# Kernel optimization log

Hardware: AMD Instinct MI355X
Metric: run time of the kernel (lower is better)

The kernel has to match this reference:

```python
import jax, jax.numpy as jnp
import numpy as np

N = 100000   # nodes
R = 8        # relations
E = 150000   # edges per relation
D_IN = 128
D_OUT = 128
B = 2        # num_bases


def setup_inputs() -> dict:
    key = jax.random.key(0)
    ks = jax.random.split(key, 7)
    return {
        "x": jax.random.normal(ks[0], (N, D_IN), dtype=jnp.float32),
        "src": jax.random.randint(ks[1], (R, E), 0, N, dtype=jnp.int32),
        "dst": jax.random.randint(ks[2], (R, E), 0, N, dtype=jnp.int32),
        "basis_coeff": jax.random.normal(ks[3], (R, B), dtype=jnp.float32),
        "bases": jax.random.normal(ks[4], (B, D_IN, D_OUT), dtype=jnp.float32) * 0.05,
        "loop_weight": jax.random.normal(ks[5], (D_IN, D_OUT), dtype=jnp.float32) * 0.05,
        "h_bias": jax.random.normal(ks[6], (D_OUT,), dtype=jnp.float32) * 0.01,
    }


def reference(x, src, dst, basis_coeff, bases, loop_weight, h_bias):
    n = x.shape[0]
    # basis-decomposed per-relation weights: [R, D_IN, D_OUT]
    weight = jnp.einsum('rb,bio->rio', basis_coeff, bases)
    # gather src features per relation: [R, E, D_IN]
    msgs = x[src]
    # scatter-add onto dst nodes per relation (SpMM aggregate): [R, N, D_IN]
    agg = jax.vmap(lambda m, d: jax.ops.segment_sum(m, d, num_segments=n))(msgs, dst)
    # right normalization: divide by in-degree (clamped to 1), as in DGL GraphConv norm='right'
    ones = jnp.ones(src.shape[1], dtype=x.dtype)
    deg = jax.vmap(lambda d: jax.ops.segment_sum(ones, d, num_segments=n))(dst)
    agg = agg / jnp.clip(deg, 1.0)[..., None]
    # per-relation weight then sum across relations (HeteroGraphConv 'sum' agg)
    h = jnp.einsum('rni,rio->no', agg, weight)
    # self-loop + bias + activation (dropout = 0.0, eval)
    h = h + x @ loop_weight + h_bias
    return jax.nn.relu(h)
```

## Files before the change

### kernel.cpp

```cpp
#include <hip/hip_runtime.h>
#include <hip/hip_fp16.h>


#define DFEAT 128
#define NREL 8
#define ALDA 264
#define ECAP 1024

typedef __attribute__((ext_vector_type(8))) short bf16x8;
typedef __attribute__((ext_vector_type(4))) float f32x4;
typedef __attribute__((ext_vector_type(2))) float f32x2;

__device__ __forceinline__ ushort f2bf(float f) {
    unsigned u = __float_as_uint(f);
    u += 0x7FFF + ((u >> 16) & 1);
    return (ushort)(u >> 16);
}
__device__ __forceinline__ float bflo(unsigned u) { return __uint_as_float(u << 16); }
__device__ __forceinline__ float bfhi(unsigned u) { return __uint_as_float(u & 0xFFFF0000u); }
__device__ __forceinline__ unsigned pack2bf(float lo, float hi) {
    return (unsigned)f2bf(lo) | ((unsigned)f2bf(hi) << 16);
}

__global__ void fused_pre(const int* __restrict__ dst, int* __restrict__ deg,
                          ushort* __restrict__ rank,
                          const float* __restrict__ x, ushort* __restrict__ xb,
                          const float* __restrict__ bases, const float* __restrict__ loopw,
                          ushort* __restrict__ w2T,
                          int RE, int E, int N, int n4) {
    const int stride = gridDim.x * blockDim.x;
    const int t0 = blockIdx.x * blockDim.x + threadIdx.x;
    for (int i = t0; i < RE; i += stride) {
        int r = i / E;
        int d = dst[i];
        rank[i] = (ushort)atomicAdd(&deg[r * N + d], 1);
    }
    for (int i = t0; i < n4; i += stride) {
        float4 v = ((const float4*)x)[i];
        ushort4 o;
        o.x = f2bf(v.x); o.y = f2bf(v.y); o.z = f2bf(v.z); o.w = f2bf(v.w);
        ((ushort4*)xb)[i] = o;
    }
    for (int i = t0; i < 128 * 384; i += stride) {
        int j = i / 384, k = i % 384;
        float v = (k < 256) ? bases[(k >> 7) * DFEAT * DFEAT + (k & 127) * DFEAT + j]
                            : loopw[(k - 256) * DFEAT + j];
        w2T[i] = f2bf(v);
    }
}

__global__ void scan_block_sums(const int* __restrict__ deg, int* __restrict__ cnt,
                                int* __restrict__ bsums, int N) {
    __shared__ int sdata[256];
    int b = blockIdx.x, t = threadIdx.x;
    int idx = b * 256 + t;
    int sum = 0;
    if (idx < N) {
        #pragma unroll
        for (int r = 0; r < NREL; ++r) sum += deg[r * N + idx];
        cnt[idx] = sum;
    }
    sdata[t] = sum; __syncthreads();
    for (int s = 128; s > 0; s >>= 1) {
        if (t < s) sdata[t] += sdata[t + s];
        __syncthreads();
    }
    if (t == 0) bsums[b] = sdata[0];
}

__global__ void scan_write(const int* __restrict__ cnt, const int* __restrict__ bsums,
                           const int* __restrict__ deg,
                           int* __restrict__ rowStart, unsigned* __restrict__ packed,
                           int N) {
    __shared__ int sdata[256];
    int b = blockIdx.x, t = threadIdx.x;

    int part = 0;
    for (int k = t; k < b; k += 256) part += bsums[k];
    sdata[t] = part; __syncthreads();
    for (int s = 128; s > 0; s >>= 1) {
        if (t < s) sdata[t] += sdata[t + s];
        __syncthreads();
    }
    const int boff = sdata[0];
    __syncthreads();

    int idx = b * 256 + t;
    int c = (idx < N) ? cnt[idx] : 0;
    sdata[t] = c; __syncthreads();
    for (int off = 1; off < 256; off <<= 1) {
        int x = 0;
        if (t >= off) x = sdata[t - off];
        __syncthreads();
        if (t >= off) sdata[t] += x;
        __syncthreads();
    }
    int excl = sdata[t] - c;
    if (idx < N) {
        int rs = boff + excl;
        rowStart[idx] = rs;
        int pre = 0;
        #pragma unroll
        for (int r = 0; r < NREL; ++r) {
            int dv = deg[r * N + idx];
            packed[r * N + idx] = ((unsigned)(rs + pre) << 11) | (unsigned)dv;
            pre += dv;
        }
    }
}

__global__ void fill_kernel(const int* __restrict__ src, const int* __restrict__ dst,
                            const float* __restrict__ coeff,
                            const ushort* __restrict__ rank,
                            const unsigned* __restrict__ packed,
                            uint2* __restrict__ recs, int RE, int E, int N) {
    int idx = blockIdx.x * blockDim.x + threadIdx.x;
    if (idx >= RE) return;
    int r = idx / E;
    int d = dst[idx];
    unsigned p = packed[r * N + d];
    int pos = (int)(p >> 11) + (int)rank[idx];
    float inv = 1.0f / (float)(p & 2047u);
    __half2 hc = __floats2half2_rn(coeff[2 * r] * inv, coeff[2 * r + 1] * inv);
    uint2 rec;
    rec.x = (unsigned)src[idx];
    rec.y = *(unsigned*)&hc;
    recs[pos] = rec;
}

__global__ __launch_bounds__(256, 5) void gather_gemm(
    const uint2* __restrict__ recs, const int* __restrict__ rowStart,
    const ushort* __restrict__ xb,
    const ushort* __restrict__ w2T, const float* __restrict__ bias,
    float* __restrict__ out, int N, int RE) {
    __shared__ __align__(16) ushort agg[32 * ALDA];
    __shared__ __align__(16) uint2 recsL[ECAP];
    __shared__ int rsl[33];
    const int tid = threadIdx.x;
    const int wave = tid >> 6, lane = tid & 63;
    const int row0 = blockIdx.x * 32;

    if (tid < 33) {
        int d = row0 + tid;
        rsl[tid] = (d < N) ? rowStart[d] : RE;
    }
    __syncthreads();
    const int e0 = rsl[0];
    const int cntE = rsl[32] - e0;
    const bool fits = (cntE <= ECAP);
    {
        const int lim = fits ? cntE : 0;
        for (int k = tid; k < lim; k += 256)
            recsL[k] = recs[e0 + k];
    }
    __syncthreads();

    {
        const int qw = tid >> 4;
        const int h  = tid & 15;

        auto gatherNode = [&](int i, auto getRec) {
            const int s   = rsl[i] - e0;
            const int len = rsl[i + 1] - rsl[i];
            f32x2 A0 = {0.f,0.f}, A1 = {0.f,0.f}, A2 = {0.f,0.f}, A3 = {0.f,0.f};
            f32x2 B0 = {0.f,0.f}, B1 = {0.f,0.f}, B2 = {0.f,0.f}, B3 = {0.f,0.f};
            if (len > 0) {
                const int last = s + len - 1;
                for (int k = 0; k < len; k += 8) {
                    uint2 rc[8];
                    #pragma unroll
                    for (int j = 0; j < 8; ++j) {
                        int li = s + k + j;
                        rc[j] = getRec(li <= last ? li : last);
                    }
                    uint4 u[8];
                    #pragma unroll
                    for (int j = 0; j < 8; ++j)
                        u[j] = *(const uint4*)(xb + (size_t)rc[j].x * DFEAT + h * 8);
                    #pragma unroll
                    for (int j = 0; j < 8; ++j) {
                        bool v = (k + j) < len;
                        __half2 hc = *(__half2*)&rc[j].y;
                        float c0 = v ? __low2float(hc) : 0.f;
                        float c1 = v ? __high2float(hc) : 0.f;
                        f32x2 cc0 = {c0, c0}, cc1 = {c1, c1};
                        uint4 uu = u[j];
                        f32x2 f01 = {bflo(uu.x), bfhi(uu.x)};
                        f32x2 f23 = {bflo(uu.y), bfhi(uu.y)};
                        f32x2 f45 = {bflo(uu.z), bfhi(uu.z)};
                        f32x2 f67 = {bflo(uu.w), bfhi(uu.w)};
                        A0 += cc0 * f01; A1 += cc0 * f23; A2 += cc0 * f45; A3 += cc0 * f67;
                        B0 += cc1 * f01; B1 += cc1 * f23; B2 += cc1 * f45; B3 += cc1 * f67;
                    }
                }
            }
            uint4 w0, w1;
            w0.x = pack2bf(A0.x, A0.y); w0.y = pack2bf(A1.x, A1.y);
            w0.z = pack2bf(A2.x, A2.y); w0.w = pack2bf(A3.x, A3.y);
            w1.x = pack2bf(B0.x, B0.y); w1.y = pack2bf(B1.x, B1.y);
            w1.z = pack2bf(B2.x, B2.y); w1.w = pack2bf(B3.x, B3.y);
            *(uint4*)(agg + i * ALDA + h * 8)       = w0;
            *(uint4*)(agg + i * ALDA + 128 + h * 8) = w1;
        };

        if (fits) {
            #pragma unroll
            for (int p = 0; p < 2; ++p)
                gatherNode(qw + p * 16, [&](int li) { return recsL[li]; });
        } else {
            #pragma unroll
            for (int p = 0; p < 2; ++p)
                gatherNode(qw + p * 16, [&](int li) { return recs[e0 + li]; });
        }
    }
    __syncthreads();

    const int quad = lane >> 4, l16 = lane & 15;
    int arow[2];
    #pragma unroll
    for (int m = 0; m < 2; ++m) {
        int r = row0 + m * 16 + l16;
        arow[m] = (r < N) ? r : 0;
    }

    f32x4 zero = {0.f, 0.f, 0.f, 0.f};
    f32x4 acc[2][2] = {{zero, zero}, {zero, zero}};

    #pragma unroll
    for (int kt = 0; kt < 3; ++kt) {
        bf16x8 bq[4][2];
        #pragma unroll
        for (int t = 0; t < 4; ++t)
            #pragma unroll
            for (int g = 0; g < 2; ++g)
                bq[t][g] = *(const bf16x8*)(w2T + (size_t)(wave * 32 + g * 16 + l16) * 384
                                            + kt * 128 + t * 32 + quad * 8);
        #pragma unroll
        for (int m = 0; m < 2; ++m) {
            #pragma unroll
            for (int t = 0; t < 4; ++t) {
                bf16x8 a;
                if (kt < 2)
                    a = *(const bf16x8*)(agg + (m * 16 + l16) * ALDA + kt * 128 + t * 32 + quad * 8);
                else
                    a = *(const bf16x8*)(xb + (size_t)arow[m] * DFEAT + t * 32 + quad * 8);
                acc[m][0] = __builtin_amdgcn_mfma_f32_16x16x32_bf16(a, bq[t][0], acc[m][0], 0, 0, 0);
                acc[m][1] = __builtin_amdgcn_mfma_f32_16x16x32_bf16(a, bq[t][1], acc[m][1], 0, 0, 0);
            }
        }
    }

    #pragma unroll
    for (int g = 0; g < 2; ++g) {
        int c = wave * 32 + g * 16 + l16;
        float bv = bias[c];
        #pragma unroll
        for (int m = 0; m < 2; ++m) {
            #pragma unroll
            for (int reg = 0; reg < 4; ++reg) {
                int grow = row0 + m * 16 + quad * 4 + reg;
                if (grow < N)
                    out[(size_t)grow * DFEAT + c] = fmaxf(acc[m][g][reg] + bv, 0.f);
            }
        }
    }
}

extern "C" void kernel_launch(void* const* d_in, const int* in_sizes, int n_in,
                              void* d_out, int out_size, void* d_ws, size_t ws_size,
                              hipStream_t stream) {
    const float* x     = (const float*)d_in[0];
    const int*   src   = (const int*)  d_in[1];
    const int*   dst   = (const int*)  d_in[2];
    const float* coeff = (const float*)d_in[3];
    const float* bases = (const float*)d_in[4];
    const float* loopw = (const float*)d_in[5];
    const float* bias  = (const float*)d_in[6];
    float* out = (float*)d_out;

    const int N  = in_sizes[0] / DFEAT;
    const int RE = in_sizes[1];
    const int B  = in_sizes[4] / (DFEAT * DFEAT);
    const int R  = in_sizes[3] / B;
    const int E  = RE / R;
    const int NB = (N + 255) / 256;
    const int n4 = N * 32;

    char* ws = (char*)d_ws;
    size_t off = 0;
    auto alloc = [&](size_t bytes) { void* p = ws + off; off = (off + bytes + 255) & ~(size_t)255; return p; };
    int*      deg      = (int*)     alloc((size_t)R * N * sizeof(int));
    ushort*   rank     = (ushort*)  alloc((size_t)RE * sizeof(ushort));
    unsigned* packed   = (unsigned*)alloc((size_t)R * N * sizeof(unsigned));
    int*      cnt      = (int*)     alloc((size_t)N * sizeof(int));
    int*      rowStart = (int*)     alloc((size_t)N * sizeof(int));
    int*      bsums    = (int*)     alloc((size_t)NB * sizeof(int));
    ushort*   w2T      = (ushort*)  alloc((size_t)128 * 384 * sizeof(ushort));
    ushort*   xb       = (ushort*)  alloc((size_t)N * DFEAT * sizeof(ushort));
    uint2*    recs     = (uint2*)   alloc((size_t)RE * sizeof(uint2));

    hipMemsetAsync(deg, 0, (size_t)R * N * sizeof(int), stream);
    fused_pre<<<4096, 256, 0, stream>>>(dst, deg, rank, x, xb, bases, loopw, w2T,
                                        RE, E, N, n4);
    scan_block_sums<<<NB, 256, 0, stream>>>(deg, cnt, bsums, N);
    scan_write<<<NB, 256, 0, stream>>>(cnt, bsums, deg, rowStart, packed, N);
    fill_kernel<<<(RE + 255) / 256, 256, 0, stream>>>(src, dst, coeff, rank, packed,
                                                      recs, RE, E, N);
    gather_gemm<<<(N + 31) / 32, 256, 0, stream>>>(recs, rowStart, xb, w2T,
                                                   bias, out, N, RE);
}
```

Before: 281.5 us.

## Compress edge records to 4 bytes and compute per-node coefficients in gather kernel

Edge records shrink from 8 bytes (src plus half2 coefficient) to 4 bytes, packing src (17 bits) and relation id. The per-relation normalized coefficients are computed once per destination node in shared memory inside the gather kernel, using degree and basis_coeff. The cnt array is removed and scan_write recomputes the row sums from deg, and launch bounds rise to 6 blocks. This cuts record bandwidth and the fill kernel's work, at the cost of an extra shared-memory lookup per edge and a 17-bit limit on node index that holds for N=100000.

```diff
diff --git a/kernel.cpp b/kernel.cpp
--- a/kernel.cpp
+++ b/kernel.cpp
@@ -49,7 +49,7 @@
     }
 }
 
-__global__ void scan_block_sums(const int* __restrict__ deg, int* __restrict__ cnt,
+__global__ void scan_block_sums(const int* __restrict__ deg,
                                 int* __restrict__ bsums, int N) {
     __shared__ int sdata[256];
     int b = blockIdx.x, t = threadIdx.x;
@@ -58,7 +58,6 @@
     if (idx < N) {
         #pragma unroll
         for (int r = 0; r < NREL; ++r) sum += deg[r * N + idx];
-        cnt[idx] = sum;
     }
     sdata[t] = sum; __syncthreads();
     for (int s = 128; s > 0; s >>= 1) {
@@ -68,7 +67,7 @@
     if (t == 0) bsums[b] = sdata[0];
 }
 
-__global__ void scan_write(const int* __restrict__ cnt, const int* __restrict__ bsums,
+__global__ void scan_write(const int* __restrict__ bsums,
                            const int* __restrict__ deg,
                            int* __restrict__ rowStart, unsigned* __restrict__ packed,
                            int N) {
@@ -86,7 +85,12 @@
     __syncthreads();
 
     int idx = b * 256 + t;
-    int c = (idx < N) ? cnt[idx] : 0;
+    int dvs[NREL];
+    int c = 0;
+    if (idx < N) {
+        #pragma unroll
+        for (int r = 0; r < NREL; ++r) { dvs[r] = deg[r * N + idx]; c += dvs[r]; }
+    }
     sdata[t] = c; __syncthreads();
     for (int off = 1; off < 256; off <<= 1) {
         int x = 0;
@@ -102,7 +106,7 @@
         int pre = 0;
         #pragma unroll
         for (int r = 0; r < NREL; ++r) {
-            int dv = deg[r * N + idx];
+            int dv = dvs[r];
             packed[r * N + idx] = ((unsigned)(rs + pre) << 11) | (unsigned)dv;
             pre += dv;
         }
@@ -110,31 +114,27 @@
 }
 
 __global__ void fill_kernel(const int* __restrict__ src, const int* __restrict__ dst,
-                            const float* __restrict__ coeff,
                             const ushort* __restrict__ rank,
                             const unsigned* __restrict__ packed,
-                            uint2* __restrict__ recs, int RE, int E, int N) {
+                            unsigned* __restrict__ recs, int RE, int E, int N) {
     int idx = blockIdx.x * blockDim.x + threadIdx.x;
     if (idx >= RE) return;
     int r = idx / E;
     int d = dst[idx];
     unsigned p = packed[r * N + d];
     int pos = (int)(p >> 11) + (int)rank[idx];
-    float inv = 1.0f / (float)(p & 2047u);
-    __half2 hc = __floats2half2_rn(coeff[2 * r] * inv, coeff[2 * r + 1] * inv);
-    uint2 rec;
-    rec.x = (unsigned)src[idx];
-    rec.y = *(unsigned*)&hc;
-    recs[pos] = rec;
-}
-
-__global__ __launch_bounds__(256, 5) void gather_gemm(
-    const uint2* __restrict__ recs, const int* __restrict__ rowStart,
+    recs[pos] = (unsigned)src[idx] | ((unsigned)r << 17);
+}
+
+__global__ __launch_bounds__(256, 6) void gather_gemm(
+    const unsigned* __restrict__ recs, const int* __restrict__ rowStart,
+    const int* __restrict__ deg, const float* __restrict__ coeff,
     const ushort* __restrict__ xb,
     const ushort* __restrict__ w2T, const float* __restrict__ bias,
     float* __restrict__ out, int N, int RE) {
     __shared__ __align__(16) ushort agg[32 * ALDA];
-    __shared__ __align__(16) uint2 recsL[ECAP];
+    __shared__ __align__(16) unsigned recsL[ECAP];
+    __shared__ float2 ccL[32 * NREL];
     __shared__ int rsl[33];
     const int tid = threadIdx.x;
     const int wave = tid >> 6, lane = tid & 63;
@@ -143,6 +143,18 @@
     if (tid < 33) {
         int d = row0 + tid;
         rsl[tid] = (d < N) ? rowStart[d] : RE;
+    }
+    {
+        int i = tid & 31, r = tid >> 5;
+        int d = row0 + i;
+        float2 cc = {0.f, 0.f};
+        if (d < N) {
+            int dv = deg[r * N + d];
+            float inv = (dv > 0) ? 1.0f / (float)dv : 0.f;
+            cc.x = coeff[2 * r] * inv;
+            cc.y = coeff[2 * r + 1] * inv;
+        }
+        ccL[i * NREL + r] = cc;
     }
     __syncthreads();
     const int e0 = rsl[0];
@@ -167,7 +179,7 @@
             if (len > 0) {
                 const int last = s + len - 1;
                 for (int k = 0; k < len; k += 8) {
-                    uint2 rc[8];
+                    unsigned rc[8];
                     #pragma unroll
                     for (int j = 0; j < 8; ++j) {
                         int li = s + k + j;
@@ -176,13 +188,13 @@
                     uint4 u[8];
                     #pragma unroll
                     for (int j = 0; j < 8; ++j)
-                        u[j] = *(const uint4*)(xb + (size_t)rc[j].x * DFEAT + h * 8);
+                        u[j] = *(const uint4*)(xb + (size_t)(rc[j] & 0x1FFFFu) * DFEAT + h * 8);
                     #pragma unroll
                     for (int j = 0; j < 8; ++j) {
                         bool v = (k + j) < len;
-                        __half2 hc = *(__half2*)&rc[j].y;
-                        float c0 = v ? __low2float(hc) : 0.f;
-                        float c1 = v ? __high2float(hc) : 0.f;
+                        float2 cf = ccL[i * NREL + (rc[j] >> 17)];
+                        float c0 = v ? cf.x : 0.f;
+                        float c1 = v ? cf.y : 0.f;
                         f32x2 cc0 = {c0, c0}, cc1 = {c1, c1};
                         uint4 uu = u[j];
                         f32x2 f01 = {bflo(uu.x), bfhi(uu.x)};
@@ -292,20 +304,19 @@
     int*      deg      = (int*)     alloc((size_t)R * N * sizeof(int));
     ushort*   rank     = (ushort*)  alloc((size_t)RE * sizeof(ushort));
     unsigned* packed   = (unsigned*)alloc((size_t)R * N * sizeof(unsigned));
-    int*      cnt      = (int*)     alloc((size_t)N * sizeof(int));
     int*      rowStart = (int*)     alloc((size_t)N * sizeof(int));
     int*      bsums    = (int*)     alloc((size_t)NB * sizeof(int));
     ushort*   w2T      = (ushort*)  alloc((size_t)128 * 384 * sizeof(ushort));
     ushort*   xb       = (ushort*)  alloc((size_t)N * DFEAT * sizeof(ushort));
-    uint2*    recs     = (uint2*)   alloc((size_t)RE * sizeof(uint2));
+    unsigned* recs     = (unsigned*)alloc((size_t)RE * sizeof(unsigned));
 
     hipMemsetAsync(deg, 0, (size_t)R * N * sizeof(int), stream);
     fused_pre<<<4096, 256, 0, stream>>>(dst, deg, rank, x, xb, bases, loopw, w2T,
                                         RE, E, N, n4);
-    scan_block_sums<<<NB, 256, 0, stream>>>(deg, cnt, bsums, N);
-    scan_write<<<NB, 256, 0, stream>>>(cnt, bsums, deg, rowStart, packed, N);
-    fill_kernel<<<(RE + 255) / 256, 256, 0, stream>>>(src, dst, coeff, rank, packed,
+    scan_block_sums<<<NB, 256, 0, stream>>>(deg, bsums, N);
+    scan_write<<<NB, 256, 0, stream>>>(bsums, deg, rowStart, packed, N);
+    fill_kernel<<<(RE + 255) / 256, 256, 0, stream>>>(src, dst, rank, packed,
                                                       recs, RE, E, N);
-    gather_gemm<<<(N + 31) / 32, 256, 0, stream>>>(recs, rowStart, xb, w2T,
-                                                   bias, out, N, RE);
-}
+    gather_gemm<<<(N + 31) / 32, 256, 0, stream>>>(recs, rowStart, deg, coeff,
+                                                   xb, w2T, bias, out, N, RE);
+}
```

Measured after the change: 282.2 us. About the same (+0.2%).
